# Kernel optimization log

Measured on AMD Instinct MI355X. Metric: run time of the kernel, lower is better.

Reference implementation:

```python
import jax, jax.numpy as jnp
import numpy as np

N = 100000      # nodes
E = 1600000     # edges
IN_FEATS = 128
HIDDEN = 64
NUM_GRAPHS = 512
BN_EPS = 1e-5


def setup_inputs() -> dict:
    key = jax.random.key(0)
    ks = jax.random.split(key, 20)
    x = jax.random.normal(ks[0], (N, IN_FEATS), dtype=jnp.float32)
    edge_index = jax.random.randint(ks[1], (2, E), 0, N, dtype=jnp.int64)
    batch = jnp.sort(jax.random.randint(ks[2], (N,), 0, NUM_GRAPHS, dtype=jnp.int64))
    def lin(k, fin, fout):
        k1, k2 = jax.random.split(k)
        s = 1.0 / np.sqrt(fin)
        W = jax.random.uniform(k1, (fout, fin), minval=-s, maxval=s, dtype=jnp.float32)
        b = jax.random.uniform(k2, (fout,), minval=-s, maxval=s, dtype=jnp.float32)
        return W, b
    W1a, b1a = lin(ks[3], IN_FEATS, HIDDEN)
    W1b, b1b = lin(ks[4], HIDDEN, HIDDEN)
    W2a, b2a = lin(ks[5], HIDDEN, HIDDEN)
    W2b, b2b = lin(ks[6], HIDDEN, HIDDEN)
    def bn(k):
        k1, k2, k3, k4 = jax.random.split(k, 4)
        g = jax.random.uniform(k1, (HIDDEN,), minval=0.5, maxval=1.5, dtype=jnp.float32)
        be = jax.random.normal(k2, (HIDDEN,), dtype=jnp.float32) * 0.1
        m = jax.random.normal(k3, (HIDDEN,), dtype=jnp.float32) * 0.1
        v = jax.random.uniform(k4, (HIDDEN,), minval=0.5, maxval=1.5, dtype=jnp.float32)
        return g, be, m, v
    g1, be1, m1, v1 = bn(ks[7])
    g2, be2, m2, v2 = bn(ks[8])
    return dict(x=x, edge_index=edge_index, batch=batch,
                W1a=W1a, b1a=b1a, W1b=W1b, b1b=b1b, g1=g1, be1=be1, m1=m1, v1=v1,
                W2a=W2a, b2a=b2a, W2b=W2b, b2b=b2b, g2=g2, be2=be2, m2=m2, v2=v2)


def _gin_layer(x, src, dst, Wa, ba, Wb, bb):
    # sum-aggregate neighbor features: gather at src, scatter-add to dst
    agg = jax.ops.segment_sum(x[src], dst, num_segments=N)
    h = x + agg  # eps = 0 default in PyG GINConv
    h = jax.nn.relu(h @ Wa.T + ba)
    return h @ Wb.T + bb


def _bn_eval(x, g, be, m, v):
    return (x - m) * (g * jax.lax.rsqrt(v + BN_EPS)) + be


def reference(x, edge_index, batch,
              W1a, b1a, W1b, b1b, g1, be1, m1, v1,
              W2a, b2a, W2b, b2b, g2, be2, m2, v2):
    src, dst = edge_index[0], edge_index[1]
    h = jax.nn.relu(_bn_eval(_gin_layer(x, src, dst, W1a, b1a, W1b, b1b), g1, be1, m1, v1))
    # dropout identity (eval)
    h = jax.nn.relu(_bn_eval(_gin_layer(h, src, dst, W2a, b2a, W2b, b2b), g2, be2, m2, v2))
    # global mean pool by graph id
    sums = jax.ops.segment_sum(h, batch, num_segments=NUM_GRAPHS)
    counts = jax.ops.segment_sum(jnp.ones((N,), dtype=h.dtype), batch, num_segments=NUM_GRAPHS)
    return sums / jnp.maximum(counts, 1.0)[:, None]
```

## Files before the change

kernel.cpp:

```cpp
#include <hip/hip_runtime.h>

#define BN_EPS 1e-5f
#define CHUNK 4096
#define MAXB 512

typedef __attribute__((ext_vector_type(8))) short short8v;
typedef __attribute__((ext_vector_type(4))) float f32x4;

__device__ __forceinline__ unsigned short f2bf(float f) {
    unsigned int u = __float_as_uint(f);
    u += 0x7FFF + ((u >> 16) & 1);
    return (unsigned short)(u >> 16);
}
__device__ __forceinline__ float bf2f(unsigned short h) {
    return __uint_as_float((unsigned int)h << 16);
}

__device__ __forceinline__ short8v pack8(const float* f) {
    short8v r;
#pragma unroll
    for (int i = 0; i < 8; i++) r[i] = (short)f2bf(f[i]);
    return r;
}


__global__ __launch_bounds__(256) void bin_count(const int* __restrict__ ei, int E,
                                                 int* __restrict__ bcnt, int nbuck) {
    __shared__ int h[MAXB];
    for (int i = threadIdx.x; i < nbuck; i += 256) h[i] = 0;
    __syncthreads();
    int i = blockIdx.x * 256 + threadIdx.x, stride = gridDim.x * 256;
    for (int e = i; e < E; e += stride) {
        int d = ei[E + e];
        atomicAdd(&h[d >> 8], 1);
    }
    __syncthreads();
    for (int b = threadIdx.x; b < nbuck; b += 256)
        if (h[b]) atomicAdd(&bcnt[b], h[b]);
}

__global__ __launch_bounds__(512) void scan_small(const int* __restrict__ bcnt,
                                                  int* __restrict__ boff,
                                                  int* __restrict__ bpos,
                                                  int* __restrict__ row_ptr_end,
                                                  int nbuck, int E) {
    __shared__ int wsum[8];
    int tid = threadIdx.x, lane = tid & 63, wv = tid >> 6;
    int val = (tid < nbuck) ? bcnt[tid] : 0;
    int s = val;
#pragma unroll
    for (int off = 1; off < 64; off <<= 1) {
        int t = __shfl_up(s, off, 64);
        if (lane >= off) s += t;
    }
    if (lane == 63) wsum[wv] = s;
    __syncthreads();
    if (wv == 0) {
        int t = (lane < 8) ? wsum[lane] : 0;
#pragma unroll
        for (int off = 1; off < 8; off <<= 1) {
            int u = __shfl_up(t, off, 64);
            if (lane >= off) t += u;
        }
        if (lane < 8) wsum[lane] = t;
    }
    __syncthreads();
    int excl = ((wv == 0) ? 0 : wsum[wv - 1]) + s - val;
    if (tid < nbuck) { boff[tid] = excl; bpos[tid] = excl; }
    if (tid == 0) { boff[nbuck] = E; *row_ptr_end = E; }
}

__global__ __launch_bounds__(256) void bin_scatter(const int* __restrict__ ei, int E,
                                                   int* __restrict__ bpos,
                                                   int* __restrict__ binned, int nbuck) {
    __shared__ int h[MAXB];
    __shared__ int res[MAXB];
    int base = blockIdx.x * CHUNK;
    int cnt = min(CHUNK, E - base);
    int tid = threadIdx.x;
    for (int b = tid; b < nbuck; b += 256) h[b] = 0;
    __syncthreads();
    for (int k = tid; k < cnt; k += 256) {
        int d = ei[E + base + k];
        atomicAdd(&h[d >> 8], 1);
    }
    __syncthreads();
    for (int b = tid; b < nbuck; b += 256) {
        int c = h[b];
        res[b] = c ? atomicAdd(&bpos[b], c) : 0;
        h[b] = 0;
    }
    __syncthreads();
    for (int k = tid; k < cnt; k += 256) {
        int srcv = ei[base + k];
        int d = ei[E + base + k];
        int b = d >> 8;
        int r = atomicAdd(&h[b], 1);
        binned[res[b] + r] = ((d & 255) << 17) | srcv;
    }
}

__global__ __launch_bounds__(256) void bucket_csr(const int* __restrict__ binned,
                                                  const int* __restrict__ boff,
                                                  int* __restrict__ row_ptr,
                                                  int* __restrict__ esrc, int N) {
    __shared__ int ncnt[256];
    __shared__ int npos[256];
    __shared__ int wsum[4];
    int b = blockIdx.x, tid = threadIdx.x, lane = tid & 63, wv = tid >> 6;
    int lo = boff[b], hi = boff[b + 1];
    int base_node = b << 8;
    ncnt[tid] = 0;
    __syncthreads();
    for (int i = lo + tid; i < hi; i += 256)
        atomicAdd(&ncnt[binned[i] >> 17], 1);
    __syncthreads();
    int c = ncnt[tid];
    int s = c;
#pragma unroll
    for (int off = 1; off < 64; off <<= 1) {
        int t = __shfl_up(s, off, 64);
        if (lane >= off) s += t;
    }
    if (lane == 63) wsum[wv] = s;
    __syncthreads();
    int woff = 0;
#pragma unroll
    for (int i = 0; i < 4; i++) woff += (i < wv) ? wsum[i] : 0;
    int abspos = lo + woff + (s - c);
    if (base_node + tid < N) row_ptr[base_node + tid] = abspos;
    npos[tid] = abspos;
    __syncthreads();
    for (int i = lo + tid; i < hi; i += 256) {
        int val = binned[i];
        int r = atomicAdd(&npos[val >> 17], 1);
        esrc[r] = val & 0x1FFFF;
    }
}


__global__ __launch_bounds__(256) void linear_mfma(const float* __restrict__ X,
                                                   const float* __restrict__ W,
                                                   unsigned short* __restrict__ Y, int N) {
    __shared__ short8v al[16 * 16];
    int tid = threadIdx.x, wv = tid >> 6, lane = tid & 63;
    int lr = lane & 15, lh = lane >> 4;
    short8v bw[4];
    {
        const float* wrow = W + (size_t)(wv * 16 + lr) * 128;
#pragma unroll
        for (int kk = 0; kk < 4; kk++) {
            float tmp[8];
            *(float4*)tmp = *(const float4*)(wrow + kk * 32 + lh * 8);
            *(float4*)(tmp + 4) = *(const float4*)(wrow + kk * 32 + lh * 8 + 4);
            bw[kk] = pack8(tmp);
        }
    }
    int r = tid >> 4, s = tid & 15;
    for (int nb = blockIdx.x * 16; nb < N; nb += gridDim.x * 16) {
        const float* xg = X + (size_t)(nb + r) * 128 + s * 8;
        float tmp[8];
        *(float4*)tmp = *(const float4*)xg;
        *(float4*)(tmp + 4) = *(const float4*)(xg + 4);
        al[r * 16 + (s ^ r)] = pack8(tmp);
        __syncthreads();
        f32x4 acc = {0.f, 0.f, 0.f, 0.f};
#pragma unroll
        for (int kk = 0; kk < 4; kk++) {
            short8v a = al[lr * 16 + ((kk * 4 + lh) ^ lr)];
            acc = __builtin_amdgcn_mfma_f32_16x16x32_bf16(a, bw[kk], acc, 0, 0, 0);
        }
        unsigned short* yb = Y + (size_t)nb * 64 + wv * 16 + lr;
#pragma unroll
        for (int ri = 0; ri < 4; ri++)
            yb[(size_t)(lh * 4 + ri) * 64] = f2bf(acc[ri]);
        __syncthreads();
    }
}

__global__ __launch_bounds__(256) void mlp1_mfma(const unsigned short* __restrict__ T,
        const float* __restrict__ W, const float* __restrict__ b,
        const float* __restrict__ g, const float* __restrict__ be,
        const float* __restrict__ m, const float* __restrict__ v,
        unsigned short* __restrict__ H, int N) {
    __shared__ short8v al[16 * 8];
    int tid = threadIdx.x, wv = tid >> 6, lane = tid & 63;
    int lr = lane & 15, lh = lane >> 4;
    short8v bw[2];
    {
        const float* wrow = W + (size_t)(wv * 16 + lr) * 64;
#pragma unroll
        for (int kk = 0; kk < 2; kk++) {
            float tmp[8];
            *(float4*)tmp = *(const float4*)(wrow + kk * 32 + lh * 8);
            *(float4*)(tmp + 4) = *(const float4*)(wrow + kk * 32 + lh * 8 + 4);
            bw[kk] = pack8(tmp);
        }
    }
    int col = wv * 16 + lr;
    float bias = b[col];
    float sc = g[col] * rsqrtf(v[col] + BN_EPS);
    float cc = be[col] - m[col] * sc;
    int rr = tid >> 3, ss = tid & 7;
    for (int nb = blockIdx.x * 16; nb < N; nb += gridDim.x * 16) {
        if (tid < 128) {
            const short8v* tg = (const short8v*)(T + (size_t)(nb + rr) * 64);
            al[rr * 8 + (ss ^ (rr & 7))] = tg[ss];
        }
        __syncthreads();
        f32x4 acc = {0.f, 0.f, 0.f, 0.f};
#pragma unroll
        for (int kk = 0; kk < 2; kk++) {
            short8v a = al[lr * 8 + ((kk * 4 + lh) ^ (lr & 7))];
            acc = __builtin_amdgcn_mfma_f32_16x16x32_bf16(a, bw[kk], acc, 0, 0, 0);
        }
        unsigned short* hb = H + (size_t)nb * 64 + col;
#pragma unroll
        for (int ri = 0; ri < 4; ri++) {
            float o = fmaxf((acc[ri] + bias) * sc + cc, 0.f);
            hb[(size_t)(lh * 4 + ri) * 64] = f2bf(o);
        }
        __syncthreads();
    }
}

__global__ __launch_bounds__(256) void mlp2_mfma(const unsigned short* __restrict__ T,
        const float* __restrict__ W1, const float* __restrict__ b1,
        const float* __restrict__ g, const float* __restrict__ be,
        const float* __restrict__ m, const float* __restrict__ v,
        const float* __restrict__ W2, unsigned short* __restrict__ Y, int N) {
    __shared__ short8v al[16 * 8];
    __shared__ short8v hl[16 * 8];
    int tid = threadIdx.x, wv = tid >> 6, lane = tid & 63;
    int lr = lane & 15, lh = lane >> 4;
    short8v bw1[2], bw2[2];
    {
        const float* w1r = W1 + (size_t)(wv * 16 + lr) * 64;
        const float* w2r = W2 + (size_t)(wv * 16 + lr) * 64;
#pragma unroll
        for (int kk = 0; kk < 2; kk++) {
            float tmp[8];
            *(float4*)tmp = *(const float4*)(w1r + kk * 32 + lh * 8);
            *(float4*)(tmp + 4) = *(const float4*)(w1r + kk * 32 + lh * 8 + 4);
            bw1[kk] = pack8(tmp);
            *(float4*)tmp = *(const float4*)(w2r + kk * 32 + lh * 8);
            *(float4*)(tmp + 4) = *(const float4*)(w2r + kk * 32 + lh * 8 + 4);
            bw2[kk] = pack8(tmp);
        }
    }
    int col = wv * 16 + lr;
    float bias = b1[col];
    float sc = g[col] * rsqrtf(v[col] + BN_EPS);
    float cc = be[col] - m[col] * sc;
    unsigned short* hu = (unsigned short*)hl;
    int rr = tid >> 3, ss = tid & 7;
    for (int nb = blockIdx.x * 16; nb < N; nb += gridDim.x * 16) {
        if (tid < 128) {
            const short8v* tg = (const short8v*)(T + (size_t)(nb + rr) * 64);
            al[rr * 8 + (ss ^ (rr & 7))] = tg[ss];
        }
        __syncthreads();
        f32x4 acc = {0.f, 0.f, 0.f, 0.f};
#pragma unroll
        for (int kk = 0; kk < 2; kk++) {
            short8v a = al[lr * 8 + ((kk * 4 + lh) ^ (lr & 7))];
            acc = __builtin_amdgcn_mfma_f32_16x16x32_bf16(a, bw1[kk], acc, 0, 0, 0);
        }
#pragma unroll
        for (int ri = 0; ri < 4; ri++) {
            float o = fmaxf((acc[ri] + bias) * sc + cc, 0.f);
            int row = lh * 4 + ri;
            int slot = (col >> 3) ^ (row & 7);
            hu[(row * 8 + slot) * 8 + (col & 7)] = f2bf(o);
        }
        __syncthreads();
        f32x4 acc2 = {0.f, 0.f, 0.f, 0.f};
#pragma unroll
        for (int kk = 0; kk < 2; kk++) {
            short8v a = hl[lr * 8 + ((kk * 4 + lh) ^ (lr & 7))];
            acc2 = __builtin_amdgcn_mfma_f32_16x16x32_bf16(a, bw2[kk], acc2, 0, 0, 0);
        }
        unsigned short* yb = Y + (size_t)nb * 64 + col;
#pragma unroll
        for (int ri = 0; ri < 4; ri++)
            yb[(size_t)(lh * 4 + ri) * 64] = f2bf(acc2[ri]);
        __syncthreads();
    }
}

__global__ __launch_bounds__(256) void gather_kernel(const unsigned short* __restrict__ Y,
                                                     const int* __restrict__ row_ptr,
                                                     const int* __restrict__ esrc,
                                                     const float* __restrict__ bias,
                                                     unsigned short* __restrict__ T, int N) {
    int wv = threadIdx.x >> 6, lane = threadIdx.x & 63;
    int node = blockIdx.x * 4 + wv;
    if (node >= N) return;
    float acc = bf2f(Y[(size_t)node * 64 + lane]) + bias[lane];
    int e0 = row_ptr[node], e1 = row_ptr[node + 1];
    int e = e0;
    for (; e + 8 <= e1; e += 8) {
        int s0 = esrc[e], s1 = esrc[e + 1], s2 = esrc[e + 2], s3 = esrc[e + 3];
        int s4 = esrc[e + 4], s5 = esrc[e + 5], s6 = esrc[e + 6], s7 = esrc[e + 7];
        float f0 = bf2f(Y[(size_t)s0 * 64 + lane]);
        float f1 = bf2f(Y[(size_t)s1 * 64 + lane]);
        float f2 = bf2f(Y[(size_t)s2 * 64 + lane]);
        float f3 = bf2f(Y[(size_t)s3 * 64 + lane]);
        float f4 = bf2f(Y[(size_t)s4 * 64 + lane]);
        float f5 = bf2f(Y[(size_t)s5 * 64 + lane]);
        float f6 = bf2f(Y[(size_t)s6 * 64 + lane]);
        float f7 = bf2f(Y[(size_t)s7 * 64 + lane]);
        acc += ((f0 + f1) + (f2 + f3)) + ((f4 + f5) + (f6 + f7));
    }
    for (; e < e1; e++) acc += bf2f(Y[(size_t)esrc[e] * 64 + lane]);
    T[(size_t)node * 64 + lane] = f2bf(fmaxf(acc, 0.f));
}

__global__ __launch_bounds__(256) void pool_kernel(const unsigned short* __restrict__ H,
                                                   const int* __restrict__ batch,
                                                   float* __restrict__ out, int N) {
    __shared__ float part[4][64];
    int g = blockIdx.x;
    int tid = threadIdx.x, wv = tid >> 6, lane = tid & 63;
    int lo = 0, hi = N;
    while (lo < hi) { int mid = (lo + hi) >> 1; if (batch[mid] < g) lo = mid + 1; else hi = mid; }
    int start = lo;
    hi = N;
    while (lo < hi) { int mid = (lo + hi) >> 1; if (batch[mid] < g + 1) lo = mid + 1; else hi = mid; }
    int end = lo;
    float acc = 0.f;
    for (int i = start + wv; i < end; i += 4) acc += bf2f(H[(size_t)i * 64 + lane]);
    part[wv][lane] = acc;
    __syncthreads();
    if (tid < 64) {
        float sfin = part[0][tid] + part[1][tid] + part[2][tid] + part[3][tid];
        float cnt = (float)(end - start);
        out[(size_t)g * 64 + tid] = sfin / fmaxf(cnt, 1.f);
    }
}

extern "C" void kernel_launch(void* const* d_in, const int* in_sizes, int n_in,
                              void* d_out, int out_size, void* d_ws, size_t ws_size,
                              hipStream_t stream) {
    const float* x   = (const float*)d_in[0];
    const int*   ei  = (const int*)d_in[1];
    const int*   bat = (const int*)d_in[2];
    const float* W1a = (const float*)d_in[3];
    const float* b1a = (const float*)d_in[4];
    const float* W1b = (const float*)d_in[5];
    const float* b1b = (const float*)d_in[6];
    const float* g1  = (const float*)d_in[7];
    const float* be1 = (const float*)d_in[8];
    const float* m1  = (const float*)d_in[9];
    const float* v1  = (const float*)d_in[10];
    const float* W2a = (const float*)d_in[11];
    const float* b2a = (const float*)d_in[12];
    const float* W2b = (const float*)d_in[13];
    const float* b2b = (const float*)d_in[14];
    const float* g2  = (const float*)d_in[15];
    const float* be2 = (const float*)d_in[16];
    const float* m2  = (const float*)d_in[17];
    const float* v2  = (const float*)d_in[18];
    float* out = (float*)d_out;

    int N = in_sizes[0] / 128;
    int E = in_sizes[1] / 2;
    int G = out_size / 64;
    int nbuck = (N + 255) >> 8;

    char* ws = (char*)d_ws;
    int* row_ptr = (int*)ws;
    int* bcnt = row_ptr + ((N + 1 + 3) & ~3);
    int* boff = bcnt + MAXB;
    int* bpos = boff + MAXB + 4;
    int* esrc = bpos + MAXB;
    unsigned short* bufA = (unsigned short*)(esrc + E);
    unsigned short* bufB = bufA + (size_t)N * 64;
    int* binned = (int*)bufB;

    hipMemsetAsync(bcnt, 0, MAXB * sizeof(int), stream);
    bin_count<<<512, 256, 0, stream>>>(ei, E, bcnt, nbuck);
    scan_small<<<1, 512, 0, stream>>>(bcnt, boff, bpos, row_ptr + N, nbuck, E);
    bin_scatter<<<(E + CHUNK - 1) / CHUNK, 256, 0, stream>>>(ei, E, bpos, binned, nbuck);
    bucket_csr<<<nbuck, 256, 0, stream>>>(binned, boff, row_ptr, esrc, N);

    linear_mfma<<<2048, 256, 0, stream>>>(x, W1a, bufA, N);
    gather_kernel<<<(N + 3) / 4, 256, 0, stream>>>(bufA, row_ptr, esrc, b1a, bufB, N);
    mlp2_mfma<<<2048, 256, 0, stream>>>(bufB, W1b, b1b, g1, be1, m1, v1, W2a, bufA, N);

    gather_kernel<<<(N + 3) / 4, 256, 0, stream>>>(bufA, row_ptr, esrc, b2a, bufB, N);
    mlp1_mfma<<<2048, 256, 0, stream>>>(bufB, W2b, b2b, g2, be2, m2, v2, bufA, N);

    pool_kernel<<<G, 256, 0, stream>>>(bufA, bat, out, N);
}
```

Baseline: 379.2 us.

## Store gather inputs as per-XCD feature planes and gather plane-wise

The linear and mlp2 kernels now write their bf16 outputs as 8 feature planes of 8 features each, instead of row-major 64-wide rows. A new gather_plane kernel gives each block one plane, chosen by blockIdx&7, so under round-robin block dispatch each XCD's L2 mostly serves a single ~1.6MB plane. Within a wave, 4-lane groups split the edges of 4 nodes and reduce with shuffles. The aim is to turn random 128B neighbor-row reads into cache-resident 16B reads. The risks are reliance on how the hardware dispatches blocks, extra shuffle reductions, and lane divergence when node degrees vary.

```diff
diff --git a/kernel.cpp b/kernel.cpp
--- a/kernel.cpp
+++ b/kernel.cpp
@@ -15,6 +15,8 @@
 __device__ __forceinline__ float bf2f(unsigned short h) {
     return __uint_as_float((unsigned int)h << 16);
 }
+__device__ __forceinline__ float bflo(unsigned int u) { return __uint_as_float(u << 16); }
+__device__ __forceinline__ float bfhi(unsigned int u) { return __uint_as_float(u & 0xffff0000u); }
 
 __device__ __forceinline__ short8v pack8(const float* f) {
     short8v r;
@@ -156,6 +158,8 @@
             bw[kk] = pack8(tmp);
         }
     }
+    int col = wv * 16 + lr;
+    unsigned short* yb = Y + (size_t)(col >> 3) * N * 8 + (col & 7);
     int r = tid >> 4, s = tid & 15;
     for (int nb = blockIdx.x * 16; nb < N; nb += gridDim.x * 16) {
         const float* xg = X + (size_t)(nb + r) * 128 + s * 8;
@@ -170,10 +174,9 @@
             short8v a = al[lr * 16 + ((kk * 4 + lh) ^ lr)];
             acc = __builtin_amdgcn_mfma_f32_16x16x32_bf16(a, bw[kk], acc, 0, 0, 0);
         }
-        unsigned short* yb = Y + (size_t)nb * 64 + wv * 16 + lr;
 #pragma unroll
         for (int ri = 0; ri < 4; ri++)
-            yb[(size_t)(lh * 4 + ri) * 64] = f2bf(acc[ri]);
+            yb[(size_t)(nb + lh * 4 + ri) * 8] = f2bf(acc[ri]);
         __syncthreads();
     }
 }
@@ -253,6 +256,7 @@
     float sc = g[col] * rsqrtf(v[col] + BN_EPS);
     float cc = be[col] - m[col] * sc;
     unsigned short* hu = (unsigned short*)hl;
+    unsigned short* yb = Y + (size_t)(col >> 3) * N * 8 + (col & 7);
     int rr = tid >> 3, ss = tid & 7;
     for (int nb = blockIdx.x * 16; nb < N; nb += gridDim.x * 16) {
         if (tid < 128) {
@@ -280,40 +284,86 @@
             short8v a = hl[lr * 8 + ((kk * 4 + lh) ^ (lr & 7))];
             acc2 = __builtin_amdgcn_mfma_f32_16x16x32_bf16(a, bw2[kk], acc2, 0, 0, 0);
         }
-        unsigned short* yb = Y + (size_t)nb * 64 + col;
 #pragma unroll
         for (int ri = 0; ri < 4; ri++)
-            yb[(size_t)(lh * 4 + ri) * 64] = f2bf(acc2[ri]);
-        __syncthreads();
-    }
-}
-
-__global__ __launch_bounds__(256) void gather_kernel(const unsigned short* __restrict__ Y,
-                                                     const int* __restrict__ row_ptr,
-                                                     const int* __restrict__ esrc,
-                                                     const float* __restrict__ bias,
-                                                     unsigned short* __restrict__ T, int N) {
+            yb[(size_t)(nb + lh * 4 + ri) * 8] = f2bf(acc2[ri]);
+        __syncthreads();
+    }
+}
+
+__global__ __launch_bounds__(256) void gather_plane(const unsigned short* __restrict__ Yp,
+        const int* __restrict__ row_ptr, const int* __restrict__ esrc,
+        const float* __restrict__ bias, unsigned short* __restrict__ T, int N) {
+    int b = blockIdx.x;
+    int p = b & 7;
+    int g = b >> 3;
     int wv = threadIdx.x >> 6, lane = threadIdx.x & 63;
-    int node = blockIdx.x * 4 + wv;
-    if (node >= N) return;
-    float acc = bf2f(Y[(size_t)node * 64 + lane]) + bias[lane];
-    int e0 = row_ptr[node], e1 = row_ptr[node + 1];
-    int e = e0;
-    for (; e + 8 <= e1; e += 8) {
-        int s0 = esrc[e], s1 = esrc[e + 1], s2 = esrc[e + 2], s3 = esrc[e + 3];
-        int s4 = esrc[e + 4], s5 = esrc[e + 5], s6 = esrc[e + 6], s7 = esrc[e + 7];
-        float f0 = bf2f(Y[(size_t)s0 * 64 + lane]);
-        float f1 = bf2f(Y[(size_t)s1 * 64 + lane]);
-        float f2 = bf2f(Y[(size_t)s2 * 64 + lane]);
-        float f3 = bf2f(Y[(size_t)s3 * 64 + lane]);
-        float f4 = bf2f(Y[(size_t)s4 * 64 + lane]);
-        float f5 = bf2f(Y[(size_t)s5 * 64 + lane]);
-        float f6 = bf2f(Y[(size_t)s6 * 64 + lane]);
-        float f7 = bf2f(Y[(size_t)s7 * 64 + lane]);
-        acc += ((f0 + f1) + (f2 + f3)) + ((f4 + f5) + (f6 + f7));
-    }
-    for (; e < e1; e++) acc += bf2f(Y[(size_t)esrc[e] * 64 + lane]);
-    T[(size_t)node * 64 + lane] = f2bf(fmaxf(acc, 0.f));
+    int grp = lane >> 2, fl = lane & 3;
+    const unsigned int* Y32 = (const unsigned int*)Yp + (size_t)p * N * 4;
+    float bw0 = bias[p * 8 + fl * 2 + 0];
+    float bw1 = bias[p * 8 + fl * 2 + 1];
+    int nb0 = g * 16 + wv * 4;
+    if (nb0 >= N) return;
+    int e0[4], e1[4];
+#pragma unroll
+    for (int nn = 0; nn < 4; nn++) {
+        int node = min(nb0 + nn, N - 1);
+        e0[nn] = row_ptr[node];
+        e1[nn] = row_ptr[node + 1];
+    }
+    int sA[4], sB[4];
+#pragma unroll
+    for (int nn = 0; nn < 4; nn++) {
+        int la = max(e1[nn] - 1, 0);
+        sA[nn] = esrc[min(e0[nn] + grp, la)];
+        sB[nn] = esrc[min(e0[nn] + 16 + grp, la)];
+    }
+    unsigned int uS[4], uA[4], uB[4];
+#pragma unroll
+    for (int nn = 0; nn < 4; nn++) uS[nn] = Y32[(size_t)min(nb0 + nn, N - 1) * 4 + fl];
+#pragma unroll
+    for (int nn = 0; nn < 4; nn++) uA[nn] = Y32[(size_t)sA[nn] * 4 + fl];
+#pragma unroll
+    for (int nn = 0; nn < 4; nn++) uB[nn] = Y32[(size_t)sB[nn] * 4 + fl];
+    float a0[4], a1[4];
+#pragma unroll
+    for (int nn = 0; nn < 4; nn++) {
+        bool okA = e0[nn] + grp < e1[nn];
+        bool okB = e0[nn] + 16 + grp < e1[nn];
+        a0[nn] = (okA ? bflo(uA[nn]) : 0.f) + (okB ? bflo(uB[nn]) : 0.f);
+        a1[nn] = (okA ? bfhi(uA[nn]) : 0.f) + (okB ? bfhi(uB[nn]) : 0.f);
+        if (grp == 0) { a0[nn] += bflo(uS[nn]) + bw0; a1[nn] += bfhi(uS[nn]) + bw1; }
+    }
+#pragma unroll
+    for (int nn = 0; nn < 4; nn++) {
+        for (int e = e0[nn] + 32; e < e1[nn]; e += 16) {
+            int ie = e + grp;
+            int s = esrc[min(ie, e1[nn] - 1)];
+            unsigned int u = Y32[(size_t)s * 4 + fl];
+            bool ok = ie < e1[nn];
+            a0[nn] += ok ? bflo(u) : 0.f;
+            a1[nn] += ok ? bfhi(u) : 0.f;
+        }
+    }
+#pragma unroll
+    for (int nn = 0; nn < 4; nn++) {
+#pragma unroll
+        for (int off = 4; off <= 32; off <<= 1) {
+            a0[nn] += __shfl_xor(a0[nn], off, 64);
+            a1[nn] += __shfl_xor(a1[nn], off, 64);
+        }
+    }
+    if (grp == 0) {
+#pragma unroll
+        for (int nn = 0; nn < 4; nn++) {
+            int node = nb0 + nn;
+            if (node < N) {
+                unsigned int o = (unsigned int)f2bf(fmaxf(a0[nn], 0.f))
+                               | ((unsigned int)f2bf(fmaxf(a1[nn], 0.f)) << 16);
+                ((unsigned int*)T)[(size_t)node * 32 + p * 4 + fl] = o;
+            }
+        }
+    }
 }
 
 __global__ __launch_bounds__(256) void pool_kernel(const unsigned short* __restrict__ H,
@@ -384,11 +434,13 @@
     bin_scatter<<<(E + CHUNK - 1) / CHUNK, 256, 0, stream>>>(ei, E, bpos, binned, nbuck);
     bucket_csr<<<nbuck, 256, 0, stream>>>(binned, boff, row_ptr, esrc, N);
 
+    int ngrp = (N + 15) / 16;
+
     linear_mfma<<<2048, 256, 0, stream>>>(x, W1a, bufA, N);
-    gather_kernel<<<(N + 3) / 4, 256, 0, stream>>>(bufA, row_ptr, esrc, b1a, bufB, N);
+    gather_plane<<<8 * ngrp, 256, 0, stream>>>(bufA, row_ptr, esrc, b1a, bufB, N);
     mlp2_mfma<<<2048, 256, 0, stream>>>(bufB, W1b, b1b, g1, be1, m1, v1, W2a, bufA, N);
 
-    gather_kernel<<<(N + 3) / 4, 256, 0, stream>>>(bufA, row_ptr, esrc, b2a, bufB, N);
+    gather_plane<<<8 * ngrp, 256, 0, stream>>>(bufA, row_ptr, esrc, b2a, bufB, N);
     mlp1_mfma<<<2048, 256, 0, stream>>>(bufB, W2b, b2b, g2, be2, m2, v2, bufA, N);
 
     pool_kernel<<<G, 256, 0, stream>>>(bufA, bat, out, N);
```

Result: slower. 427.6 us (+12.7%).

## Store projected features in column-plane layout and gather per plane with vector loads

Applied to the files above, without the earlier changes.

The linear and MLP kernels now write their bf16 outputs split into 8 planes of 8 columns, each plane laid out contiguously over nodes. The gather kernel is rewritten so each block handles one plane for 64 nodes, with 4 lanes per node reading 16-byte rows and reducing through shuffles. The aim is to shrink each plane's gathered working set so it fits in cache better, and to raise bytes per load. In exchange every edge index is read 8 times, and the writes from the producer kernels are more scattered.

```diff
diff --git a/kernel.cpp b/kernel.cpp
--- a/kernel.cpp
+++ b/kernel.cpp
@@ -15,6 +15,8 @@
 __device__ __forceinline__ float bf2f(unsigned short h) {
     return __uint_as_float((unsigned int)h << 16);
 }
+__device__ __forceinline__ float bflo(unsigned int u) { return __uint_as_float(u << 16); }
+__device__ __forceinline__ float bfhi(unsigned int u) { return __uint_as_float(u & 0xffff0000u); }
 
 __device__ __forceinline__ short8v pack8(const float* f) {
     short8v r;
@@ -156,6 +158,8 @@
             bw[kk] = pack8(tmp);
         }
     }
+    int col = wv * 16 + lr;
+    unsigned short* yb = Y + (size_t)(col >> 3) * N * 8 + (col & 7);
     int r = tid >> 4, s = tid & 15;
     for (int nb = blockIdx.x * 16; nb < N; nb += gridDim.x * 16) {
         const float* xg = X + (size_t)(nb + r) * 128 + s * 8;
@@ -170,10 +174,9 @@
             short8v a = al[lr * 16 + ((kk * 4 + lh) ^ lr)];
             acc = __builtin_amdgcn_mfma_f32_16x16x32_bf16(a, bw[kk], acc, 0, 0, 0);
         }
-        unsigned short* yb = Y + (size_t)nb * 64 + wv * 16 + lr;
 #pragma unroll
         for (int ri = 0; ri < 4; ri++)
-            yb[(size_t)(lh * 4 + ri) * 64] = f2bf(acc[ri]);
+            yb[(size_t)(nb + lh * 4 + ri) * 8] = f2bf(acc[ri]);
         __syncthreads();
     }
 }
@@ -253,6 +256,7 @@
     float sc = g[col] * rsqrtf(v[col] + BN_EPS);
     float cc = be[col] - m[col] * sc;
     unsigned short* hu = (unsigned short*)hl;
+    unsigned short* yb = Y + (size_t)(col >> 3) * N * 8 + (col & 7);
     int rr = tid >> 3, ss = tid & 7;
     for (int nb = blockIdx.x * 16; nb < N; nb += gridDim.x * 16) {
         if (tid < 128) {
@@ -280,40 +284,62 @@
             short8v a = hl[lr * 8 + ((kk * 4 + lh) ^ (lr & 7))];
             acc2 = __builtin_amdgcn_mfma_f32_16x16x32_bf16(a, bw2[kk], acc2, 0, 0, 0);
         }
-        unsigned short* yb = Y + (size_t)nb * 64 + col;
 #pragma unroll
         for (int ri = 0; ri < 4; ri++)
-            yb[(size_t)(lh * 4 + ri) * 64] = f2bf(acc2[ri]);
-        __syncthreads();
-    }
-}
-
-__global__ __launch_bounds__(256) void gather_kernel(const unsigned short* __restrict__ Y,
-                                                     const int* __restrict__ row_ptr,
-                                                     const int* __restrict__ esrc,
-                                                     const float* __restrict__ bias,
-                                                     unsigned short* __restrict__ T, int N) {
+            yb[(size_t)(nb + lh * 4 + ri) * 8] = f2bf(acc2[ri]);
+        __syncthreads();
+    }
+}
+
+__global__ __launch_bounds__(256) void gather_plane(const unsigned short* __restrict__ Yp,
+        const int* __restrict__ row_ptr, const int* __restrict__ esrc,
+        const float* __restrict__ bias, unsigned short* __restrict__ T, int N) {
+    int b = blockIdx.x;
+    int p = b & 7;
+    int g = b >> 3;
     int wv = threadIdx.x >> 6, lane = threadIdx.x & 63;
-    int node = blockIdx.x * 4 + wv;
-    if (node >= N) return;
-    float acc = bf2f(Y[(size_t)node * 64 + lane]) + bias[lane];
-    int e0 = row_ptr[node], e1 = row_ptr[node + 1];
-    int e = e0;
-    for (; e + 8 <= e1; e += 8) {
-        int s0 = esrc[e], s1 = esrc[e + 1], s2 = esrc[e + 2], s3 = esrc[e + 3];
-        int s4 = esrc[e + 4], s5 = esrc[e + 5], s6 = esrc[e + 6], s7 = esrc[e + 7];
-        float f0 = bf2f(Y[(size_t)s0 * 64 + lane]);
-        float f1 = bf2f(Y[(size_t)s1 * 64 + lane]);
-        float f2 = bf2f(Y[(size_t)s2 * 64 + lane]);
-        float f3 = bf2f(Y[(size_t)s3 * 64 + lane]);
-        float f4 = bf2f(Y[(size_t)s4 * 64 + lane]);
-        float f5 = bf2f(Y[(size_t)s5 * 64 + lane]);
-        float f6 = bf2f(Y[(size_t)s6 * 64 + lane]);
-        float f7 = bf2f(Y[(size_t)s7 * 64 + lane]);
-        acc += ((f0 + f1) + (f2 + f3)) + ((f4 + f5) + (f6 + f7));
-    }
-    for (; e < e1; e++) acc += bf2f(Y[(size_t)esrc[e] * 64 + lane]);
-    T[(size_t)node * 64 + lane] = f2bf(fmaxf(acc, 0.f));
+    int nsub = lane >> 2, slot = lane & 3;
+    int node = g * 64 + wv * 16 + nsub;
+    bool valid = node < N;
+    int nd = valid ? node : 0;
+    int e0 = row_ptr[nd];
+    int e1 = valid ? row_ptr[nd + 1] : e0;
+    const uint4* Yrow = (const uint4*)(Yp + (size_t)p * N * 8);
+    float a0 = 0.f, a1 = 0.f, a2 = 0.f, a3 = 0.f, a4 = 0.f, a5 = 0.f, a6 = 0.f, a7 = 0.f;
+    for (int e = e0 + slot; e < e1; e += 4) {
+        int s = esrc[e];
+        uint4 q = Yrow[s];
+        a0 += bflo(q.x); a1 += bfhi(q.x);
+        a2 += bflo(q.y); a3 += bfhi(q.y);
+        a4 += bflo(q.z); a5 += bfhi(q.z);
+        a6 += bflo(q.w); a7 += bfhi(q.w);
+    }
+#pragma unroll
+    for (int off = 1; off <= 2; off <<= 1) {
+        a0 += __shfl_xor(a0, off, 64);
+        a1 += __shfl_xor(a1, off, 64);
+        a2 += __shfl_xor(a2, off, 64);
+        a3 += __shfl_xor(a3, off, 64);
+        a4 += __shfl_xor(a4, off, 64);
+        a5 += __shfl_xor(a5, off, 64);
+        a6 += __shfl_xor(a6, off, 64);
+        a7 += __shfl_xor(a7, off, 64);
+    }
+    if (slot == 0 && valid) {
+        uint4 qs = Yrow[node];
+        float4 bl = *(const float4*)(bias + p * 8);
+        float4 bh = *(const float4*)(bias + p * 8 + 4);
+        a0 += bflo(qs.x) + bl.x; a1 += bfhi(qs.x) + bl.y;
+        a2 += bflo(qs.y) + bl.z; a3 += bfhi(qs.y) + bl.w;
+        a4 += bflo(qs.z) + bh.x; a5 += bfhi(qs.z) + bh.y;
+        a6 += bflo(qs.w) + bh.z; a7 += bfhi(qs.w) + bh.w;
+        uint4 o;
+        o.x = (unsigned int)f2bf(fmaxf(a0, 0.f)) | ((unsigned int)f2bf(fmaxf(a1, 0.f)) << 16);
+        o.y = (unsigned int)f2bf(fmaxf(a2, 0.f)) | ((unsigned int)f2bf(fmaxf(a3, 0.f)) << 16);
+        o.z = (unsigned int)f2bf(fmaxf(a4, 0.f)) | ((unsigned int)f2bf(fmaxf(a5, 0.f)) << 16);
+        o.w = (unsigned int)f2bf(fmaxf(a6, 0.f)) | ((unsigned int)f2bf(fmaxf(a7, 0.f)) << 16);
+        *(uint4*)(T + (size_t)node * 64 + p * 8) = o;
+    }
 }
 
 __global__ __launch_bounds__(256) void pool_kernel(const unsigned short* __restrict__ H,
@@ -384,11 +410,13 @@
     bin_scatter<<<(E + CHUNK - 1) / CHUNK, 256, 0, stream>>>(ei, E, bpos, binned, nbuck);
     bucket_csr<<<nbuck, 256, 0, stream>>>(binned, boff, row_ptr, esrc, N);
 
+    int ngb = (N + 63) / 64;
+
     linear_mfma<<<2048, 256, 0, stream>>>(x, W1a, bufA, N);
-    gather_kernel<<<(N + 3) / 4, 256, 0, stream>>>(bufA, row_ptr, esrc, b1a, bufB, N);
+    gather_plane<<<8 * ngb, 256, 0, stream>>>(bufA, row_ptr, esrc, b1a, bufB, N);
     mlp2_mfma<<<2048, 256, 0, stream>>>(bufB, W1b, b1b, g1, be1, m1, v1, W2a, bufA, N);
 
-    gather_kernel<<<(N + 3) / 4, 256, 0, stream>>>(bufA, row_ptr, esrc, b2a, bufB, N);
+    gather_plane<<<8 * ngb, 256, 0, stream>>>(bufA, row_ptr, esrc, b2a, bufB, N);
     mlp1_mfma<<<2048, 256, 0, stream>>>(bufB, W2b, b2b, g2, be2, m2, v2, bufA, N);
 
     pool_kernel<<<G, 256, 0, stream>>>(bufA, bat, out, N);
```

New measurement: 381.2 us. No clear change (+0.5%).
